# Kernel tuning notes

Hardware: AMD Instinct MI355X
Metric: run time of the kernel (lower is better)

The kernel has to match this reference:

```python
import jax, jax.numpy as jnp
import numpy as np

D = 256   # vec_dim
H = 8     # head_num
P = 1024  # patch_num
N = 8     # batch


def setup_inputs() -> dict:
    key = jax.random.key(0)
    ks = jax.random.split(key, 11)
    s = 0.05
    return {
        "inputs": jax.random.normal(ks[0], (N, D, P), dtype=jnp.float32),
        "pos_mat": jax.random.normal(ks[1], (1, H, P, P), dtype=jnp.float32),
        "Wk": jax.random.normal(ks[2], (H * D, D), dtype=jnp.float32) * s,
        "bk": jax.random.normal(ks[3], (H * D,), dtype=jnp.float32) * s,
        "Wq": jax.random.normal(ks[4], (H * D, D), dtype=jnp.float32) * s,
        "bq": jax.random.normal(ks[5], (H * D,), dtype=jnp.float32) * s,
        "Wv": jax.random.normal(ks[6], (H * D, D), dtype=jnp.float32) * s,
        "bv": jax.random.normal(ks[7], (H * D,), dtype=jnp.float32) * s,
        "Wo": jax.random.normal(ks[8], (D, H * D), dtype=jnp.float32) * s,
        "bo": jax.random.normal(ks[9], (D,), dtype=jnp.float32) * s,
    }


def reference(inputs, pos_mat, Wk, bk, Wq, bq, Wv, bv, Wo, bo):
    n, d, p = inputs.shape  # [N, D, P]
    h = Wk.shape[0] // d
    # 1x1 Conv1d == per-position GEMM: [H*D,D] x [N,D,P] -> [N,H*D,P] -> [N,H,D,P]
    k = (jnp.einsum('od,ndp->nop', Wk, inputs) + bk[:, None]).reshape(n, h, d, p)
    q = (jnp.einsum('od,ndp->nop', Wq, inputs) + bq[:, None]).reshape(n, h, d, p)
    v = (jnp.einsum('od,ndp->nop', Wv, inputs) + bv[:, None]).reshape(n, h, d, p)
    # attn[n,h,kpos,qpos] = K^T Q / sqrt(D), shape [N,H,P,P]
    attn = jnp.einsum('nhdk,nhdq->nhkq', k, q) / jnp.sqrt(jnp.asarray(d, inputs.dtype))
    attn = attn + pos_mat
    # NOTE: original uses Softmax(dim=2), i.e. over the KEY axis, not the last dim
    w = jax.nn.softmax(attn, axis=2)
    out = jnp.einsum('nhdk,nhkq->nhdq', v, w).reshape(n, h * d, p)
    return jnp.einsum('oi,nip->nop', Wo, out) + bo[:, None]
```

## Files before the change

kernel.cpp:

```cpp
#include <hip/hip_runtime.h>

typedef __bf16 bf16;
typedef __attribute__((ext_vector_type(8))) __bf16 bf16x8;
typedef __attribute__((ext_vector_type(4))) __bf16 bf16x4;
typedef __attribute__((ext_vector_type(2))) __bf16 bf16x2;
typedef __attribute__((ext_vector_type(4))) float f32x4;

#define MFMA16(a, b, c) __builtin_amdgcn_mfma_f32_16x16x32_bf16(a, b, c, 0, 0, 0)

__device__ __forceinline__ void gload_lds16(const void* g, void* l) {
  __builtin_amdgcn_global_load_lds(
      (const __attribute__((address_space(1))) void*)g,
      (__attribute__((address_space(3))) void*)l, 16, 0, 0);
}

constexpr int NH = 8, DD = 256, PP = 1024;

constexpr size_t WB_YT  = 33554432;
constexpr size_t WB_XB  = 67108864;
constexpr size_t WB_XBT = 71303168;
constexpr size_t WB_MB  = 75497472;
constexpr size_t WB_UB  = 76546048;
constexpr size_t WB_U   = 77594624;
constexpr size_t WB_BP  = 77602816;

constexpr int FL_PT0  = 0;
constexpr int FL_XT0  = 16384;
constexpr int FL_LRED = 0;
constexpr int FL_SZ   = 81920;

#define EXP_SHIFT 4.0f

__global__ __launch_bounds__(256, 1) void msa_mu(
    const float* __restrict__ Wk, const float* __restrict__ Wq,
    const float* __restrict__ Wo, const float* __restrict__ Wv,
    bf16* __restrict__ Mb, bf16* __restrict__ Ub) {
  __shared__ float lds[64 * 65];
  const int t = threadIdx.x;
  const int i0 = (blockIdx.x >> 1) * 64;
  const int jh = blockIdx.x & 1;
  const int h = blockIdx.y;
  const int mode = blockIdx.z;
  const int j0 = (t & 63) * 2 + jh * 128;
  const int ihalf = t >> 6;
  float acc0[16], acc1[16];
#pragma unroll
  for (int r = 0; r < 16; ++r) { acc0[r] = 0.f; acc1[r] = 0.f; }
  const float* __restrict__ W2 = (mode == 0) ? Wq : Wv;
  for (int dhc = 0; dhc < 256; dhc += 64) {
    __syncthreads();
    if (mode == 0) {
#pragma unroll
      for (int s = 0; s < 16; ++s) {
        int f = t + s * 256;
        int dh = f >> 6, ii = f & 63;
        lds[dh * 65 + ii] = Wk[(h * 256 + dhc + dh) * 256 + i0 + ii];
      }
    } else {
#pragma unroll
      for (int s = 0; s < 16; ++s) {
        int f = t + s * 256;
        int oo = f >> 6, dh = f & 63;
        lds[dh * 65 + oo] = Wo[(i0 + oo) * 2048 + h * 256 + dhc + dh];
      }
    }
    __syncthreads();
    for (int dl = 0; dl < 64; ++dl) {
      float2 wv = *reinterpret_cast<const float2*>(&W2[(h * 256 + dhc + dl) * 256 + j0]);
#pragma unroll
      for (int r = 0; r < 16; ++r) {
        float x = lds[dl * 65 + ihalf * 16 + r];
        acc0[r] = fmaf(x, wv.x, acc0[r]);
        acc1[r] = fmaf(x, wv.y, acc1[r]);
      }
    }
  }
  if (mode == 0) {
#pragma unroll
    for (int r = 0; r < 16; ++r) {
      int i = i0 + ihalf * 16 + r;
      bf16x2 v = { (__bf16)(acc0[r] * 0.0625f), (__bf16)(acc1[r] * 0.0625f) };
      *reinterpret_cast<bf16x2*>(&Mb[h * 65536 + i * 256 + j0]) = v;
    }
  } else {
#pragma unroll
    for (int r = 0; r < 16; ++r) {
      int o = i0 + ihalf * 16 + r;
      bf16x2 v = { (__bf16)acc0[r], (__bf16)acc1[r] };
      *reinterpret_cast<bf16x2*>(&Ub[o * 2048 + h * 256 + j0]) = v;
    }
  }
}

__global__ void msa_u(const float* __restrict__ Wk, const float* __restrict__ bq,
                      float* __restrict__ u) {
  __shared__ float bqs[256];
  const int h = blockIdx.x, t = threadIdx.x;
  bqs[t] = bq[h * 256 + t];
  __syncthreads();
  float acc = 0.f;
  for (int dh = 0; dh < 256; ++dh)
    acc = fmaf(Wk[(h * 256 + dh) * 256 + t], bqs[dh], acc);
  u[h * 256 + t] = acc * 0.0625f;
}

__global__ void msa_bp(const float* __restrict__ Wo, const float* __restrict__ bv,
                       const float* __restrict__ bo, float* __restrict__ bp) {
  const int o = blockIdx.x, t = threadIdx.x;
  float acc = 0.f;
  for (int f = t; f < 2048; f += 256)
    acc = fmaf(Wo[o * 2048 + f], bv[f], acc);
#pragma unroll
  for (int m = 32; m >= 1; m >>= 1) acc += __shfl_down(acc, m);
  __shared__ float part[4];
  if ((t & 63) == 0) part[t >> 6] = acc;
  __syncthreads();
  if (t == 0) bp[o] = bo[o] + part[0] + part[1] + part[2] + part[3];
}

__global__ __launch_bounds__(256, 4) void msa_cvtX(
    const float* __restrict__ X, bf16* __restrict__ Xb, bf16* __restrict__ XbT) {
  __shared__ __bf16 tl[64 * 68];
  const int t = threadIdx.x;
  const int p0 = blockIdx.x * 64, d0 = blockIdx.y * 64, n = blockIdx.z;
  const float* __restrict__ Xn = X + (size_t)n * DD * PP;
#pragma unroll
  for (int rr = 0; rr < 4; ++rr) {
    int r = (t >> 4) + rr * 16, c = (t & 15) * 4;
    float4 v = *reinterpret_cast<const float4*>(Xn + (size_t)(d0 + r) * PP + p0 + c);
    bf16x4 pk = { (__bf16)v.x, (__bf16)v.y, (__bf16)v.z, (__bf16)v.w };
    *reinterpret_cast<bf16x4*>(Xb + (size_t)n * DD * PP + (size_t)(d0 + r) * PP + p0 + c) = pk;
    *reinterpret_cast<bf16x4*>(&tl[r * 68 + c]) = pk;
  }
  __syncthreads();
#pragma unroll
  for (int rr = 0; rr < 4; ++rr) {
    int pr = (t >> 4) + rr * 16, dc = (t & 15) * 4;
    bf16x4 pk = { tl[(dc + 0) * 68 + pr], tl[(dc + 1) * 68 + pr],
                  tl[(dc + 2) * 68 + pr], tl[(dc + 3) * 68 + pr] };
    *reinterpret_cast<bf16x4*>(XbT + (size_t)n * PP * DD + (size_t)(p0 + pr) * DD + d0 + dc) = pk;
  }
}

__global__ __launch_bounds__(256, 2) void msa_flash(
    const bf16* __restrict__ XbT, const bf16* __restrict__ Xb,
    const bf16* __restrict__ Mb, const float* __restrict__ u,
    const float* __restrict__ pos, bf16* __restrict__ Yt) {
  extern __shared__ char smc[];
  const int t = threadIdx.x;
  const int lane = t & 63, w = t >> 6;
  const int g = lane >> 4, ln = lane & 15;
  const int kw = w >> 1, qw = w & 1;
  const int qt = blockIdx.x, h = blockIdx.y, n = blockIdx.z;
  const int qg0 = qt * 64, nh = n * 8 + h;
  const bf16* __restrict__ XbTn = XbT + (size_t)n * (PP * DD);
  const bf16* __restrict__ Xbn  = Xb + (size_t)n * (DD * PP);
  const bf16* __restrict__ Mh   = Mb + (size_t)h * (DD * DD);
  const float* __restrict__ posh = pos + (size_t)h * (PP * PP);
  float* lredp = (float*)(smc + FL_LRED);

  const int grl = lane >> 5;
  const int gcb = lane & 31;

  {
    bf16x8 ta[4][8];
#pragma unroll
    for (int mq = 0; mq < 4; ++mq)
#pragma unroll
      for (int s = 0; s < 8; ++s)
        ta[mq][s] = *reinterpret_cast<const bf16x8*>(
            XbTn + (size_t)(qg0 + mq * 16 + ln) * DD + s * 32 + g * 8);
#pragma unroll
    for (int ni = 0; ni < 4; ++ni) {
      const int i_ = w * 64 + ni * 16 + ln;
      bf16x8 tb8[8];
#pragma unroll
      for (int s = 0; s < 8; ++s)
        tb8[s] = *reinterpret_cast<const bf16x8*>(Mh + (size_t)i_ * DD + s * 32 + g * 8);
      const float uv = u[h * 256 + i_];
#pragma unroll
      for (int mq = 0; mq < 4; ++mq) {
        f32x4 acc = {0.f, 0.f, 0.f, 0.f};
#pragma unroll
        for (int s = 0; s < 8; ++s) acc = MFMA16(ta[mq][s], tb8[s], acc);
#pragma unroll
        for (int r = 0; r < 4; ++r) {
          const int q = mq * 16 + 4 * g + r;
          const int addr = FL_XT0 + q * 512 +
              (((w * 8 + ni * 2 + (ln >> 3)) ^ (q & 7)) << 4) + (ln & 7) * 2;
          *reinterpret_cast<__bf16*>(smc + addr) = (__bf16)(acc[r] + uv);
        }
      }
    }
  }
  __syncthreads();

  bf16x8 tb[2][8];
#pragma unroll
  for (int nq = 0; nq < 2; ++nq) {
    const int q_ = qw * 32 + nq * 16 + ln;
#pragma unroll
    for (int s = 0; s < 8; ++s)
      tb[nq][s] = *reinterpret_cast<const bf16x8*>(
          smc + FL_XT0 + q_ * 512 + (((4 * s + g) ^ (q_ & 7)) << 4));
  }
  __syncthreads();

#pragma unroll
  for (int c = 0; c < 8; ++c) {
    const int row = w * 16 + c * 2 + grl;
    const int cbg = gcb ^ (row & 7);
    gload_lds16(XbTn + (size_t)row * DD + cbg * 8,
                smc + FL_XT0 + w * 8192 + c * 1024);
  }
  __syncthreads();

  float lsum[2] = {0.f, 0.f};
  f32x4 yacc[4][4];
#pragma unroll
  for (int a = 0; a < 4; ++a)
#pragma unroll
    for (int b = 0; b < 4; ++b) { f32x4 z = {0.f, 0.f, 0.f, 0.f}; yacc[a][b] = z; }

  for (int kt = 0; kt < 16; ++kt) {
    const int kg0 = kt * 64;
    const int curXT = FL_XT0 + (kt & 1) * 32768;
    const int nxtXT = FL_XT0 + ((kt + 1) & 1) * 32768;
    const int curPT = FL_PT0 + (kt & 1) * 8192;
    if (kt < 15) {
#pragma unroll
      for (int c = 0; c < 8; ++c) {
        const int row = w * 16 + c * 2 + grl;
        const int cbg = gcb ^ (row & 7);
        gload_lds16(XbTn + (size_t)(kg0 + 64 + row) * DD + cbg * 8,
                    smc + nxtXT + w * 8192 + c * 1024);
      }
    }
    float posv[2][2][4];
#pragma unroll
    for (int mt = 0; mt < 2; ++mt)
#pragma unroll
      for (int nq = 0; nq < 2; ++nq) {
        const float* pr = posh + (size_t)(kg0 + kw * 32 + mt * 16 + 4 * g) * PP +
                          qg0 + qw * 32 + nq * 16 + ln;
#pragma unroll
        for (int r = 0; r < 4; ++r) posv[mt][nq][r] = pr[(size_t)r * PP];
      }
    f32x4 sacc[2][2];
#pragma unroll
    for (int a = 0; a < 2; ++a)
#pragma unroll
      for (int b = 0; b < 2; ++b) { f32x4 z = {0.f, 0.f, 0.f, 0.f}; sacc[a][b] = z; }
#pragma unroll
    for (int mt = 0; mt < 2; ++mt) {
      const int row = kw * 32 + mt * 16 + ln;
      bf16x8 af8[8];
#pragma unroll
      for (int s = 0; s < 8; ++s)
        af8[s] = *reinterpret_cast<const bf16x8*>(
            smc + curXT + row * 512 + (((4 * s + g) ^ (row & 7)) << 4));
#pragma unroll
      for (int s = 0; s < 8; ++s)
#pragma unroll
        for (int nq = 0; nq < 2; ++nq)
          sacc[mt][nq] = MFMA16(af8[s], tb[nq][s], sacc[mt][nq]);
    }
#pragma unroll
    for (int mt = 0; mt < 2; ++mt)
#pragma unroll
      for (int nq = 0; nq < 2; ++nq) {
        bf16x4 pk;
#pragma unroll
        for (int r = 0; r < 4; ++r) {
          float e = __expf(sacc[mt][nq][r] + posv[mt][nq][r] - EXP_SHIFT);
          lsum[nq] += e;
          pk[r] = (__bf16)e;
        }
        const int q_ = qw * 32 + nq * 16 + ln;
        *reinterpret_cast<bf16x4*>(smc + curPT + q_ * 128 +
            (((kw * 4 + mt * 2 + (g >> 1)) ^ (q_ & 7)) << 4) + ((g & 1) << 3)) = pk;
      }
    __syncthreads();
#pragma unroll
    for (int ks = 0; ks < 2; ++ks) {
      bf16x8 pa[4], xv[4];
#pragma unroll
      for (int mq = 0; mq < 4; ++mq) {
        const int q_ = mq * 16 + ln;
        pa[mq] = *reinterpret_cast<const bf16x8*>(
            smc + curPT + q_ * 128 + (((4 * ks + g) ^ (q_ & 7)) << 4));
      }
#pragma unroll
      for (int nd = 0; nd < 4; ++nd)
        xv[nd] = *reinterpret_cast<const bf16x8*>(
            Xbn + (size_t)(w * 64 + nd * 16 + ln) * PP + kg0 + ks * 32 + g * 8);
#pragma unroll
      for (int mq = 0; mq < 4; ++mq)
#pragma unroll
        for (int nd = 0; nd < 4; ++nd)
          yacc[mq][nd] = MFMA16(pa[mq], xv[nd], yacc[mq][nd]);
    }
  }

#pragma unroll
  for (int nq = 0; nq < 2; ++nq) {
    lsum[nq] += __shfl_xor(lsum[nq], 16);
    lsum[nq] += __shfl_xor(lsum[nq], 32);
  }
  if (lane < 16) {
#pragma unroll
    for (int nq = 0; nq < 2; ++nq)
      lredp[kw * 64 + qw * 32 + nq * 16 + ln] = lsum[nq];
  }
  __syncthreads();
  bf16* __restrict__ Ytp = Yt + (size_t)nh * (PP * DD);
#pragma unroll
  for (int mq = 0; mq < 4; ++mq) {
    f32x4 l0 = *reinterpret_cast<const f32x4*>(lredp + mq * 16 + 4 * g);
    f32x4 l1 = *reinterpret_cast<const f32x4*>(lredp + 64 + mq * 16 + 4 * g);
    f32x4 inv;
#pragma unroll
    for (int r = 0; r < 4; ++r) inv[r] = 1.0f / (l0[r] + l1[r]);
#pragma unroll
    for (int nd = 0; nd < 4; ++nd)
#pragma unroll
      for (int r = 0; r < 4; ++r)
        Ytp[(size_t)(qg0 + mq * 16 + 4 * g + r) * DD + w * 64 + nd * 16 + ln] =
            (__bf16)(yacc[mq][nd][r] * inv[r]);
  }
}

__global__ __launch_bounds__(256, 3) void msa_final4(
    const bf16* __restrict__ Ub, const bf16* __restrict__ Yt,
    const float* __restrict__ bp, float* __restrict__ out) {
  __shared__ char lsd[49152];
  const int t = threadIdx.x, lane = t & 63, w = t >> 6;
  const int g = lane >> 4, ln = lane & 15;
  const int pw = w & 1, ow = w >> 1;
  const int pb = blockIdx.x * 128, ob = blockIdx.y * 64, n = blockIdx.z;
  const bf16* __restrict__ Ytn = Yt + (size_t)n * 8 * (PP * DD);
  f32x4 acc[2][4];
#pragma unroll
  for (int a = 0; a < 2; ++a)
#pragma unroll
    for (int b = 0; b < 4; ++b) { f32x4 z = {0.f, 0.f, 0.f, 0.f}; acc[a][b] = z; }

  uint4 areg[2], breg[4];
  {
#pragma unroll
    for (int j = 0; j < 2; ++j) {
      int u_ = t + j * 256;
      areg[j] = *reinterpret_cast<const uint4*>(
          Ub + (size_t)(ob + (u_ >> 3)) * 2048 + 0 + (u_ & 7) * 8);
    }
#pragma unroll
    for (int j = 0; j < 4; ++j) {
      int v_ = t + j * 256;
      breg[j] = *reinterpret_cast<const uint4*>(
          Ytn + ((size_t)0 * PP + pb + (v_ >> 3)) * DD + 0 + (v_ & 7) * 8);
    }
#pragma unroll
    for (int j = 0; j < 2; ++j) {
      int u_ = t + j * 256, row = u_ >> 3, cb = u_ & 7;
      *reinterpret_cast<uint4*>(lsd + row * 128 + ((cb ^ (row & 7)) << 4)) = areg[j];
    }
#pragma unroll
    for (int j = 0; j < 4; ++j) {
      int v_ = t + j * 256, row = v_ >> 3, cb = v_ & 7;
      *reinterpret_cast<uint4*>(lsd + 8192 + row * 128 + ((cb ^ (row & 7)) << 4)) = breg[j];
    }
  }
  __syncthreads();

  for (int kc = 0; kc < 32; ++kc) {
    const int cur = (kc & 1) * 24576;
    const int nxt = ((kc + 1) & 1) * 24576;
    if (kc < 31) {
      const int k1 = (kc + 1) * 64, hh = k1 >> 8, dd = k1 & 255;
#pragma unroll
      for (int j = 0; j < 2; ++j) {
        int u_ = t + j * 256;
        areg[j] = *reinterpret_cast<const uint4*>(
            Ub + (size_t)(ob + (u_ >> 3)) * 2048 + k1 + (u_ & 7) * 8);
      }
#pragma unroll
      for (int j = 0; j < 4; ++j) {
        int v_ = t + j * 256;
        breg[j] = *reinterpret_cast<const uint4*>(
            Ytn + ((size_t)hh * PP + pb + (v_ >> 3)) * DD + dd + (v_ & 7) * 8);
      }
    }
#pragma unroll
    for (int ks = 0; ks < 2; ++ks) {
      bf16x8 a[2], b[4];
#pragma unroll
      for (int mo = 0; mo < 2; ++mo) {
        const int row = ow * 32 + mo * 16 + ln;
        a[mo] = *reinterpret_cast<const bf16x8*>(
            lsd + cur + row * 128 + (((4 * ks + g) ^ (row & 7)) << 4));
      }
#pragma unroll
      for (int np = 0; np < 4; ++np) {
        const int row = pw * 64 + np * 16 + ln;
        b[np] = *reinterpret_cast<const bf16x8*>(
            lsd + cur + 8192 + row * 128 + (((4 * ks + g) ^ (row & 7)) << 4));
      }
#pragma unroll
      for (int mo = 0; mo < 2; ++mo)
#pragma unroll
        for (int np = 0; np < 4; ++np) acc[mo][np] = MFMA16(a[mo], b[np], acc[mo][np]);
    }
    if (kc < 31) {
#pragma unroll
      for (int j = 0; j < 2; ++j) {
        int u_ = t + j * 256, row = u_ >> 3, cb = u_ & 7;
        *reinterpret_cast<uint4*>(lsd + nxt + row * 128 + ((cb ^ (row & 7)) << 4)) = areg[j];
      }
#pragma unroll
      for (int j = 0; j < 4; ++j) {
        int v_ = t + j * 256, row = v_ >> 3, cb = v_ & 7;
        *reinterpret_cast<uint4*>(lsd + nxt + 8192 + row * 128 + ((cb ^ (row & 7)) << 4)) = breg[j];
      }
    }
    __syncthreads();
  }

#pragma unroll
  for (int mo = 0; mo < 2; ++mo) {
    f32x4 bv = *reinterpret_cast<const f32x4*>(bp + ob + ow * 32 + mo * 16 + 4 * g);
#pragma unroll
    for (int np = 0; np < 4; ++np)
#pragma unroll
      for (int r = 0; r < 4; ++r) {
        const int o = ob + ow * 32 + mo * 16 + 4 * g + r;
        out[((size_t)n * DD + o) * PP + pb + pw * 64 + np * 16 + ln] =
            acc[mo][np][r] + bv[r];
      }
  }
}

extern "C" void kernel_launch(void* const* d_in, const int* in_sizes, int n_in,
                              void* d_out, int out_size, void* d_ws, size_t ws_size,
                              hipStream_t stream) {
  const float* X   = (const float*)d_in[0];
  const float* pos = (const float*)d_in[1];
  const float* Wk  = (const float*)d_in[2];
  const float* Wq  = (const float*)d_in[4];
  const float* bq  = (const float*)d_in[5];
  const float* Wv  = (const float*)d_in[6];
  const float* bv  = (const float*)d_in[7];
  const float* Wo  = (const float*)d_in[8];
  const float* bo  = (const float*)d_in[9];

  char* ws = (char*)d_ws;
  bf16* Yt  = (bf16*)(ws + WB_YT);
  bf16* Xb  = (bf16*)(ws + WB_XB);
  bf16* XbT = (bf16*)(ws + WB_XBT);
  bf16* Mb  = (bf16*)(ws + WB_MB);
  bf16* Ub  = (bf16*)(ws + WB_UB);
  float* u  = (float*)(ws + WB_U);
  float* bp = (float*)(ws + WB_BP);
  float* out = (float*)d_out;

  hipFuncSetAttribute(reinterpret_cast<const void*>(msa_flash),
                      hipFuncAttributeMaxDynamicSharedMemorySize, FL_SZ);

  msa_cvtX<<<dim3(16, 4, 8), 256, 0, stream>>>(X, Xb, XbT);
  msa_mu<<<dim3(8, 8, 2), 256, 0, stream>>>(Wk, Wq, Wo, Wv, Mb, Ub);
  msa_u<<<8, 256, 0, stream>>>(Wk, bq, u);
  msa_bp<<<256, 256, 0, stream>>>(Wo, bv, bo, bp);
  msa_flash<<<dim3(16, 8, 8), 256, FL_SZ, stream>>>(XbT, Xb, Mb, u, pos, Yt);
  msa_final4<<<dim3(8, 4, 8), 256, 0, stream>>>(Ub, Yt, bp, out);
}
```

Baseline: 282.5 us.

## Fold bias-vector precompute kernels into weight-product kernel and widen its grid

Removes the separate msa_u and msa_bp launches and computes the u = Wk·bq and per-head Wo·bv partial bias vectors inside msa_mu, using the weight tiles already staged in shared memory. The msa_mu grid doubles by splitting the output columns into quarters with fewer accumulators per thread, which raises parallelism for this weight-only preprocessing. The final kernel now sums the eight per-head partial biases plus bo in its epilogue. This saves two kernel launches and redundant weight reads, at the cost of a small extra reduction in the final kernel and some idle threads in msa_mu.

Result: faster. 269.3 us (-4.7%).

```diff
diff --git a/kernel.cpp b/kernel.cpp
--- a/kernel.cpp
+++ b/kernel.cpp
@@ -22,7 +22,7 @@
 constexpr size_t WB_MB  = 75497472;
 constexpr size_t WB_UB  = 76546048;
 constexpr size_t WB_U   = 77594624;
-constexpr size_t WB_BP  = 77602816;
+constexpr size_t WB_BPP = 77602816;
 
 constexpr int FL_PT0  = 0;
 constexpr int FL_XT0  = 16384;
@@ -34,19 +34,24 @@
 __global__ __launch_bounds__(256, 1) void msa_mu(
     const float* __restrict__ Wk, const float* __restrict__ Wq,
     const float* __restrict__ Wo, const float* __restrict__ Wv,
-    bf16* __restrict__ Mb, bf16* __restrict__ Ub) {
+    const float* __restrict__ bq, const float* __restrict__ bv,
+    bf16* __restrict__ Mb, bf16* __restrict__ Ub,
+    float* __restrict__ u, float* __restrict__ bpp) {
   __shared__ float lds[64 * 65];
+  __shared__ float svec[64];
   const int t = threadIdx.x;
-  const int i0 = (blockIdx.x >> 1) * 64;
-  const int jh = blockIdx.x & 1;
+  const int i0 = (blockIdx.x >> 2) * 64;
+  const int jq = blockIdx.x & 3;
   const int h = blockIdx.y;
   const int mode = blockIdx.z;
-  const int j0 = (t & 63) * 2 + jh * 128;
-  const int ihalf = t >> 6;
-  float acc0[16], acc1[16];
-#pragma unroll
-  for (int r = 0; r < 16; ++r) { acc0[r] = 0.f; acc1[r] = 0.f; }
+  const int j0 = (t & 31) * 2 + jq * 64;
+  const int i8 = t >> 5;
+  float acc0[8], acc1[8];
+#pragma unroll
+  for (int r = 0; r < 8; ++r) { acc0[r] = 0.f; acc1[r] = 0.f; }
+  float accS = 0.f;
   const float* __restrict__ W2 = (mode == 0) ? Wq : Wv;
+  const float* __restrict__ vec = (mode == 0) ? bq : bv;
   for (int dhc = 0; dhc < 256; dhc += 64) {
     __syncthreads();
     if (mode == 0) {
@@ -64,58 +69,41 @@
         lds[dh * 65 + oo] = Wo[(i0 + oo) * 2048 + h * 256 + dhc + dh];
       }
     }
+    if (jq == 0 && t < 64) svec[t] = vec[h * 256 + dhc + t];
     __syncthreads();
     for (int dl = 0; dl < 64; ++dl) {
-      float2 wv = *reinterpret_cast<const float2*>(&W2[(h * 256 + dhc + dl) * 256 + j0]);
-#pragma unroll
-      for (int r = 0; r < 16; ++r) {
-        float x = lds[dl * 65 + ihalf * 16 + r];
-        acc0[r] = fmaf(x, wv.x, acc0[r]);
-        acc1[r] = fmaf(x, wv.y, acc1[r]);
-      }
+      float2 wv2 = *reinterpret_cast<const float2*>(&W2[(h * 256 + dhc + dl) * 256 + j0]);
+#pragma unroll
+      for (int r = 0; r < 8; ++r) {
+        float x = lds[dl * 65 + i8 * 8 + r];
+        acc0[r] = fmaf(x, wv2.x, acc0[r]);
+        acc1[r] = fmaf(x, wv2.y, acc1[r]);
+      }
+    }
+    if (jq == 0 && t < 64) {
+      float a = 0.f;
+#pragma unroll 8
+      for (int dh = 0; dh < 64; ++dh) a = fmaf(lds[dh * 65 + t], svec[dh], a);
+      accS += a;
     }
   }
   if (mode == 0) {
 #pragma unroll
-    for (int r = 0; r < 16; ++r) {
-      int i = i0 + ihalf * 16 + r;
+    for (int r = 0; r < 8; ++r) {
+      int i = i0 + i8 * 8 + r;
       bf16x2 v = { (__bf16)(acc0[r] * 0.0625f), (__bf16)(acc1[r] * 0.0625f) };
       *reinterpret_cast<bf16x2*>(&Mb[h * 65536 + i * 256 + j0]) = v;
     }
+    if (jq == 0 && t < 64) u[h * 256 + i0 + t] = accS * 0.0625f;
   } else {
 #pragma unroll
-    for (int r = 0; r < 16; ++r) {
-      int o = i0 + ihalf * 16 + r;
+    for (int r = 0; r < 8; ++r) {
+      int o = i0 + i8 * 8 + r;
       bf16x2 v = { (__bf16)acc0[r], (__bf16)acc1[r] };
       *reinterpret_cast<bf16x2*>(&Ub[o * 2048 + h * 256 + j0]) = v;
     }
-  }
-}
-
-__global__ void msa_u(const float* __restrict__ Wk, const float* __restrict__ bq,
-                      float* __restrict__ u) {
-  __shared__ float bqs[256];
-  const int h = blockIdx.x, t = threadIdx.x;
-  bqs[t] = bq[h * 256 + t];
-  __syncthreads();
-  float acc = 0.f;
-  for (int dh = 0; dh < 256; ++dh)
-    acc = fmaf(Wk[(h * 256 + dh) * 256 + t], bqs[dh], acc);
-  u[h * 256 + t] = acc * 0.0625f;
-}
-
-__global__ void msa_bp(const float* __restrict__ Wo, const float* __restrict__ bv,
-                       const float* __restrict__ bo, float* __restrict__ bp) {
-  const int o = blockIdx.x, t = threadIdx.x;
-  float acc = 0.f;
-  for (int f = t; f < 2048; f += 256)
-    acc = fmaf(Wo[o * 2048 + f], bv[f], acc);
-#pragma unroll
-  for (int m = 32; m >= 1; m >>= 1) acc += __shfl_down(acc, m);
-  __shared__ float part[4];
-  if ((t & 63) == 0) part[t >> 6] = acc;
-  __syncthreads();
-  if (t == 0) bp[o] = bo[o] + part[0] + part[1] + part[2] + part[3];
+    if (jq == 0 && t < 64) bpp[h * 256 + i0 + t] = accS;
+  }
 }
 
 __global__ __launch_bounds__(256, 4) void msa_cvtX(
@@ -332,7 +320,8 @@
 
 __global__ __launch_bounds__(256, 3) void msa_final4(
     const bf16* __restrict__ Ub, const bf16* __restrict__ Yt,
-    const float* __restrict__ bp, float* __restrict__ out) {
+    const float* __restrict__ bo, const float* __restrict__ bpp,
+    float* __restrict__ out) {
   __shared__ char lsd[49152];
   const int t = threadIdx.x, lane = t & 63, w = t >> 6;
   const int g = lane >> 4, ln = lane & 15;
@@ -427,14 +416,21 @@
 
 #pragma unroll
   for (int mo = 0; mo < 2; ++mo) {
-    f32x4 bv = *reinterpret_cast<const f32x4*>(bp + ob + ow * 32 + mo * 16 + 4 * g);
+    const int o4 = ob + ow * 32 + mo * 16 + 4 * g;
+    f32x4 bb = *reinterpret_cast<const f32x4*>(bo + o4);
+#pragma unroll
+    for (int hh = 0; hh < 8; ++hh) {
+      f32x4 pv = *reinterpret_cast<const f32x4*>(bpp + hh * 256 + o4);
+#pragma unroll
+      for (int r = 0; r < 4; ++r) bb[r] += pv[r];
+    }
 #pragma unroll
     for (int np = 0; np < 4; ++np)
 #pragma unroll
       for (int r = 0; r < 4; ++r) {
-        const int o = ob + ow * 32 + mo * 16 + 4 * g + r;
+        const int o = o4 + r;
         out[((size_t)n * DD + o) * PP + pb + pw * 64 + np * 16 + ln] =
-            acc[mo][np][r] + bv[r];
+            acc[mo][np][r] + bb[r];
       }
   }
 }
@@ -459,16 +455,14 @@
   bf16* Mb  = (bf16*)(ws + WB_MB);
   bf16* Ub  = (bf16*)(ws + WB_UB);
   float* u  = (float*)(ws + WB_U);
-  float* bp = (float*)(ws + WB_BP);
+  float* bpp = (float*)(ws + WB_BPP);
   float* out = (float*)d_out;
 
   hipFuncSetAttribute(reinterpret_cast<const void*>(msa_flash),
                       hipFuncAttributeMaxDynamicSharedMemorySize, FL_SZ);
 
   msa_cvtX<<<dim3(16, 4, 8), 256, 0, stream>>>(X, Xb, XbT);
-  msa_mu<<<dim3(8, 8, 2), 256, 0, stream>>>(Wk, Wq, Wo, Wv, Mb, Ub);
-  msa_u<<<8, 256, 0, stream>>>(Wk, bq, u);
-  msa_bp<<<256, 256, 0, stream>>>(Wo, bv, bo, bp);
+  msa_mu<<<dim3(16, 8, 2), 256, 0, stream>>>(Wk, Wq, Wo, Wv, bq, bv, Mb, Ub, u, bpp);
   msa_flash<<<dim3(16, 8, 8), 256, FL_SZ, stream>>>(XbT, Xb, Mb, u, pos, Yt);
-  msa_final4<<<dim3(8, 4, 8), 256, 0, stream>>>(Ub, Yt, bp, out);
-}
+  msa_final4<<<dim3(8, 4, 8), 256, 0, stream>>>(Ub, Yt, bo, bpp, out);
+}
```
